# Performance work log

Hardware: AMD Instinct MI355X
Metric: run time of the kernel (lower is better)

The kernel has to match this reference:

```python
import jax, jax.numpy as jnp
import numpy as np

NUM_CLASSES = 2
BG_PID = 5532
NUM_ROIS = 128          # cfg.TRAIN.BATCH_SIZE
NUM_FG_MAX = 32         # round(cfg.TRAIN.FG_FRACTION * BATCH_SIZE), FG_FRACTION = 0.25
FG_THRESH = 0.5
BG_THRESH_HI = 0.5
BG_THRESH_LO = 0.1
MEANS = jnp.array([0.0, 0.0, 0.0, 0.0], dtype=jnp.float32)
STDS = jnp.array([0.1, 0.1, 0.2, 0.2], dtype=jnp.float32)
INSIDE_W = jnp.array([1.0, 1.0, 1.0, 1.0], dtype=jnp.float32)


def _make_boxes(key, n, img_w=1000.0, img_h=600.0):
    k1, k2, k3, k4 = jax.random.split(key, 4)
    x1 = jax.random.uniform(k1, (n,)) * (img_w - 330.0)
    y1 = jax.random.uniform(k2, (n,)) * (img_h - 350.0)
    w = 20.0 + jax.random.uniform(k3, (n,)) * 300.0
    h = 40.0 + jax.random.uniform(k4, (n,)) * 300.0
    return jnp.stack([x1, y1, x1 + w, y1 + h], axis=1).astype(jnp.float32)


def setup_inputs() -> dict:
    key = jax.random.key(0)
    kr, kg, kp = jax.random.split(key, 3)
    R, G = 131072, 256
    rois = _make_boxes(kr, R)
    all_rois = jnp.concatenate([jnp.zeros((R, 1), jnp.float32), rois], axis=1)  # [R,5]
    gtb = _make_boxes(kg, G)
    labels = jnp.ones((G, 1), jnp.float32)  # person class = 1
    pids = jax.random.randint(kp, (G, 1), 0, BG_PID).astype(jnp.float32)
    gt_boxes = jnp.concatenate([gtb, labels, pids], axis=1)  # [G,6]
    return {"all_rois": all_rois, "gt_boxes": gt_boxes}


def bbox_overlaps(a, b):
    iw = jnp.minimum(a[:, None, 2], b[None, :, 2]) - jnp.maximum(a[:, None, 0], b[None, :, 0]) + 1.0
    ih = jnp.minimum(a[:, None, 3], b[None, :, 3]) - jnp.maximum(a[:, None, 1], b[None, :, 1]) + 1.0
    iw = jnp.maximum(iw, 0.0)
    ih = jnp.maximum(ih, 0.0)
    area_a = (a[:, 2] - a[:, 0] + 1.0) * (a[:, 3] - a[:, 1] + 1.0)
    area_b = (b[:, 2] - b[:, 0] + 1.0) * (b[:, 3] - b[:, 1] + 1.0)
    inter = iw * ih
    return inter / (area_a[:, None] + area_b[None, :] - inter)


def bbox_transform(ex, gt):
    ew = ex[:, 2] - ex[:, 0] + 1.0
    eh = ex[:, 3] - ex[:, 1] + 1.0
    ecx = ex[:, 0] + 0.5 * ew
    ecy = ex[:, 1] + 0.5 * eh
    gw = gt[:, 2] - gt[:, 0] + 1.0
    gh = gt[:, 3] - gt[:, 1] + 1.0
    gcx = gt[:, 0] + 0.5 * gw
    gcy = gt[:, 1] + 0.5 * gh
    return jnp.stack([(gcx - ecx) / ew, (gcy - ecy) / eh,
                      jnp.log(gw / ew), jnp.log(gh / eh)], axis=1)


def _forward(all_rois, gt_boxes):
    G = gt_boxes.shape[0]
    gt_rois = jnp.concatenate([jnp.zeros((G, 1), all_rois.dtype), gt_boxes[:, :4]], axis=1)
    rois_all = jnp.concatenate([all_rois, gt_rois], axis=0)  # [R+G,5]
    N = rois_all.shape[0]
    overlaps = bbox_overlaps(rois_all[:, 1:5], gt_boxes[:, :4])  # [R+G, G]
    argmax_ov = jnp.argmax(overlaps, axis=1)
    max_ov = jnp.max(overlaps, axis=1)
    labels_all = gt_boxes[argmax_ov, 4]
    pids_all = gt_boxes[argmax_ov, 5]
    fg_mask = max_ov >= FG_THRESH
    bg_mask = (max_ov < BG_THRESH_HI) & (max_ov >= BG_THRESH_LO)
    num_fg = jnp.minimum(jnp.int32(NUM_FG_MAX), fg_mask.sum().astype(jnp.int32))
    num_bg = jnp.minimum(jnp.int32(NUM_ROIS) - num_fg, bg_mask.sum().astype(jnp.int32))
    # deterministic 'take first k' selection (DEBUG path of the original),
    # expressed as a fixed-shape scatter: rank within fg/bg -> output slot
    fg_rank = (jnp.cumsum(fg_mask) - 1).astype(jnp.int32)
    bg_rank = (jnp.cumsum(bg_mask) - 1).astype(jnp.int32)
    idx = jnp.arange(N, dtype=jnp.int32)
    pos_fg = jnp.where(fg_mask & (fg_rank < num_fg), fg_rank, jnp.int32(NUM_ROIS))
    pos_bg = jnp.where(bg_mask & (bg_rank < num_bg), num_fg + bg_rank, jnp.int32(NUM_ROIS))
    keep = jnp.zeros((NUM_ROIS,), jnp.int32)
    keep = keep.at[pos_fg].set(idx, mode="drop")
    keep = keep.at[pos_bg].set(idx, mode="drop")
    slot_is_fg = jnp.arange(NUM_ROIS) < num_fg
    rois = rois_all[keep]                                   # [128,5]
    labels = jnp.where(slot_is_fg, labels_all[keep], 0.0)
    pids = jnp.where(slot_is_fg, pids_all[keep], jnp.float32(BG_PID))
    tgt = bbox_transform(rois[:, 1:5], gt_boxes[argmax_ov[keep], :4])
    tgt = (tgt - MEANS) / STDS
    cls = jnp.round(labels).astype(jnp.int32)
    onehot = jax.nn.one_hot(cls, NUM_CLASSES, dtype=tgt.dtype) * (labels > 0).astype(tgt.dtype)[:, None]
    bbox_targets = (onehot[:, :, None] * tgt[:, None, :]).reshape(NUM_ROIS, 4 * NUM_CLASSES)
    bbox_inside = (onehot[:, :, None] * INSIDE_W[None, None, :]).reshape(NUM_ROIS, 4 * NUM_CLASSES)
    bbox_outside = (onehot[:, :, None] * jnp.ones((4,), tgt.dtype)).reshape(NUM_ROIS, 4 * NUM_CLASSES)
    return rois, labels, pids, bbox_targets, bbox_inside, bbox_outside


def reference(all_rois, gt_boxes):
    rois, labels, pids, bt, bi, bo = _forward(all_rois, gt_boxes)
    return rois, labels.astype(jnp.int32), pids.astype(jnp.int32), bt, bi, bo
```

## Files before the change

kernel.cpp:

```cpp
#include <hip/hip_runtime.h>
#include <stdint.h>

#define OUT_ROIS 128
#define FG_MAX 32
#define BG_PID_F 5532.0f
#define MAXCH 2304

#define MFG_D ((double)0x1FFFFFF / (double)(1 << 26))
#define MBG_D (26843545.0 / 268435456.0)

__global__ __launch_bounds__(512, 8) void ptl_classify(
    const float* __restrict__ all_rois, const float* __restrict__ gt,
    int R, int G, int N,
    uint8_t* __restrict__ code, int* __restrict__ blkF, int* __restrict__ blkB)
{
#pragma clang fp contract(off)
    __shared__ float4 g4[256];
    __shared__ float  gA[256];
    __shared__ uint32_t flg[4][128];
    const int t = threadIdx.x;
    const int w = t >> 6, lane = t & 63;
    const int q = w >> 1, half = w & 1;

    if (t < G) {
        const float* p = gt + (size_t)t * 6;
        const float a = p[0], b = p[1], c = p[2], d = p[3];
        g4[t] = make_float4(a, b, c, d);
        gA[t] = ((c - a) + 1.0f) * ((d - b) + 1.0f);
    }
    __syncthreads();

    const int rl = half * 64 + lane;
    const int i = blockIdx.x * 128 + rl;
    float x1, y1, x2, y2;
    if (i < N) {
        if (i < R) {
            const float* p = all_rois + (size_t)i * 5;
            x1 = p[1]; y1 = p[2]; x2 = p[3]; y2 = p[4];
        } else {
            const float* p = gt + (size_t)(i - R) * 6;
            x1 = p[0]; y1 = p[1]; x2 = p[2]; y2 = p[3];
        }
    } else { x1 = 0.0f; y1 = 0.0f; x2 = -2.0f; y2 = -2.0f; }
    const float A = ((x2 - x1) + 1.0f) * ((y2 - y1) + 1.0f);

    const int jbeg = (G * q) >> 2;
    const int jend = (G * (q + 1)) >> 2;
    double tF = 1.0, tB = 1.0;
#pragma unroll 8
    for (int j = jbeg; j < jend; ++j) {
        const float4 qq = g4[j];
        const float ga = gA[j];
        float iw = (fminf(x2, qq.z) - fmaxf(x1, qq.x)) + 1.0f;
        float ih = (fminf(y2, qq.w) - fmaxf(y1, qq.y)) + 1.0f;
        iw = fmaxf(iw, 0.0f);
        ih = fmaxf(ih, 0.0f);
        const float inter = iw * ih;
        const float den = (A + ga) - inter;
        const double i64 = (double)inter, d64 = (double)den;
        tF = fmin(tF, fma(MFG_D, d64, -i64));
        tB = fmin(tB, fma(MBG_D, d64, -i64));
    }
    flg[q][rl] = (tF <= 0.0 ? 1u : 0u) | (tB < 0.0 ? 2u : 0u);
    __syncthreads();

    if (t < 128) {
        const uint32_t u = flg[0][t] | flg[1][t] | flg[2][t] | flg[3][t];
        const int cls = (u & 1u) ? 1 : ((u & 2u) ? 2 : 0);
        const int i2 = blockIdx.x * 128 + t;
        if (i2 < N) code[i2] = (uint8_t)cls;
        unsigned long long mF = __ballot(cls == 1);
        unsigned long long mB = __ballot(cls == 2);
        if ((t & 63) == 0) {
            blkF[blockIdx.x * 2 + (t >> 6)] = __popcll(mF);
            blkB[blockIdx.x * 2 + (t >> 6)] = __popcll(mB);
        }
    }
}

__global__ __launch_bounds__(256) void ptl_select_emit(
    const float* __restrict__ all_rois, const float* __restrict__ gt,
    const uint8_t* __restrict__ code,
    const int* __restrict__ blkF, const int* __restrict__ blkB,
    int R, int G, int N, int nch,
    float* __restrict__ out)
{
#pragma clang fp contract(off)
    __shared__ int sF[MAXCH], sB[MAXCH];
    __shared__ int EF[MAXCH], EB[MAXCH];
    __shared__ int tsF[256], tsB[256];
    __shared__ int keep[OUT_ROIS];
    __shared__ int sam[OUT_ROIS];
    __shared__ int nwork;
    __shared__ unsigned short work[MAXCH];
    const int t = threadIdx.x;

    for (int c = t; c < nch; c += 256) { sF[c] = blkF[c]; sB[c] = blkB[c]; }
    for (int c = nch + t; c < MAXCH; c += 256) { sF[c] = 0; sB[c] = 0; }
    if (t < OUT_ROIS) { keep[t] = 0; sam[t] = 0; }
    if (t == 0) nwork = 0;
    __syncthreads();

    const int c0 = t * (MAXCH / 256);
    int baseF = 0, baseB = 0;
#pragma unroll
    for (int k = 0; k < MAXCH / 256; ++k) { baseF += sF[c0 + k]; baseB += sB[c0 + k]; }
    tsF[t] = baseF; tsB[t] = baseB;
    __syncthreads();
    for (int d = 1; d < 256; d <<= 1) {
        int vF = (t >= d) ? tsF[t - d] : 0;
        int vB = (t >= d) ? tsB[t - d] : 0;
        __syncthreads();
        tsF[t] += vF; tsB[t] += vB;
        __syncthreads();
    }
    const int tf = tsF[255], tb = tsB[255];
    const int num_fg = tf < FG_MAX ? tf : FG_MAX;
    const int rem = OUT_ROIS - num_fg;
    const int num_bg = tb < rem ? tb : rem;

    int rF = tsF[t] - baseF, rB = tsB[t] - baseB;
#pragma unroll
    for (int k = 0; k < MAXCH / 256; ++k) {
        const int c = c0 + k;
        const int cf = sF[c], cb = sB[c];
        EF[c] = rF; EB[c] = rB;
        const bool need = ((cf > 0 && rF < num_fg) || (cb > 0 && rB < num_bg)) && (c < nch);
        if (need) { int p = atomicAdd(&nwork, 1); work[p] = (unsigned short)c; }
        rF += cf; rB += cb;
    }
    __syncthreads();

    const int w = t >> 6, lane = t & 63;
    const unsigned long long lowmask = (1ull << lane) - 1ull;
    const int nw = nwork;
    for (int idx = w; idx < nw; idx += 4) {
        const int c = work[idx];
        const int i = c * 64 + lane;
        const int cd = (i < N) ? (int)code[i] : 0;
        unsigned long long mF = __ballot(cd == 1);
        unsigned long long mB = __ballot(cd == 2);
        const int pF = EF[c] + __popcll(mF & lowmask);
        const int pB = EB[c] + __popcll(mB & lowmask);
        if (cd == 1 && pF < num_fg) keep[pF] = i;
        if (cd == 2 && pB < num_bg) keep[num_fg + pB] = i;
    }
    __syncthreads();

    for (int s = w; s < num_fg; s += 4) {
        const int k = keep[s];
        float x1, y1, x2, y2;
        if (k < R) {
            const float* p = all_rois + (size_t)k * 5;
            x1 = p[1]; y1 = p[2]; x2 = p[3]; y2 = p[4];
        } else {
            const float* p = gt + (size_t)(k - R) * 6;
            x1 = p[0]; y1 = p[1]; x2 = p[2]; y2 = p[3];
        }
        const float A = ((x2 - x1) + 1.0f) * ((y2 - y1) + 1.0f);
        float mv = -1.0f; int mj = 0;
        for (int jj = 0; jj < 4; ++jj) {
            const int j = jj * 64 + lane;
            float iou = -1.0f;
            if (j < G) {
                const float* p = gt + (size_t)j * 6;
                const float a = p[0], b = p[1], c2 = p[2], d2 = p[3];
                const float ga = ((c2 - a) + 1.0f) * ((d2 - b) + 1.0f);
                float iw = (fminf(x2, c2) - fmaxf(x1, a)) + 1.0f;
                float ih = (fminf(y2, d2) - fmaxf(y1, b)) + 1.0f;
                iw = fmaxf(iw, 0.0f);
                ih = fmaxf(ih, 0.0f);
                const float inter = iw * ih;
                iou = inter / ((A + ga) - inter);
            }
            if (iou > mv) { mv = iou; mj = j; }
        }
#pragma unroll
        for (int m = 1; m < 64; m <<= 1) {
            const float ov = __shfl_xor(mv, m);
            const int oj = __shfl_xor(mj, m);
            if (ov > mv || (ov == mv && oj < mj)) { mv = ov; mj = oj; }
        }
        if (lane == 0) sam[s] = mj;
    }
    __syncthreads();

    if (t < OUT_ROIS) {
        const int s = t;
        const int k = keep[s];
        const bool isfg = s < num_fg;
        float x1, y1, x2, y2;
        if (k < R) {
            const float* p = all_rois + (size_t)k * 5;
            x1 = p[1]; y1 = p[2]; x2 = p[3]; y2 = p[4];
        } else {
            const float* p = gt + (size_t)(k - R) * 6;
            x1 = p[0]; y1 = p[1]; x2 = p[2]; y2 = p[3];
        }
        const int amax = sam[s];
        const float* g = gt + (size_t)amax * 6;
        const float gx1v = g[0], gy1v = g[1], gx2v = g[2], gy2v = g[3];
        const float label = isfg ? g[4] : 0.0f;
        const float pid = isfg ? g[5] : BG_PID_F;

        float* ro = out + (size_t)s * 5;
        ro[0] = 0.0f; ro[1] = x1; ro[2] = y1; ro[3] = x2; ro[4] = y2;
        out[640 + s] = (float)(int)label;
        out[768 + s] = (float)(int)pid;

        const float ew = (x2 - x1) + 1.0f, eh = (y2 - y1) + 1.0f;
        const float ecx = x1 + 0.5f * ew, ecy = y1 + 0.5f * eh;
        const float gw = (gx2v - gx1v) + 1.0f, gh = (gy2v - gy1v) + 1.0f;
        const float gcx = gx1v + 0.5f * gw, gcy = gy1v + 0.5f * gh;
        float tv[4];
        tv[0] = ((gcx - ecx) / ew) / 0.1f;
        tv[1] = ((gcy - ecy) / eh) / 0.1f;
        tv[2] = logf(gw / ew) / 0.2f;
        tv[3] = logf(gh / eh) / 0.2f;

        const int cls = (int)roundf(label);
        const float on = (label > 0.0f) ? 1.0f : 0.0f;

        float* bt = out + 896  + (size_t)s * 8;
        float* bi = out + 1920 + (size_t)s * 8;
        float* bo = out + 2944 + (size_t)s * 8;
#pragma unroll
        for (int cc = 0; cc < 2; ++cc) {
            const float sel = (cc == cls) ? on : 0.0f;
#pragma unroll
            for (int j = 0; j < 4; ++j) {
                bt[cc * 4 + j] = sel * tv[j];
                bi[cc * 4 + j] = sel;
                bo[cc * 4 + j] = sel;
            }
        }
    }
}

extern "C" void kernel_launch(void* const* d_in, const int* in_sizes, int n_in,
                              void* d_out, int out_size, void* d_ws, size_t ws_size,
                              hipStream_t stream) {
    const float* all_rois = (const float*)d_in[0];
    const float* gt       = (const float*)d_in[1];
    const int R = in_sizes[0] / 5;
    const int G = in_sizes[1] / 6;
    const int N = R + G;
    const int nblk = (N + 127) / 128;
    const int nch = (N + 63) / 64;

    uint8_t* code = (uint8_t*)d_ws;
    size_t codeBytes = ((size_t)N + 255) & ~(size_t)255;
    int* blkF = (int*)((char*)d_ws + codeBytes);
    int* blkB = blkF + 2 * nblk;
    float* out = (float*)d_out;

    ptl_classify<<<nblk, 512, 0, stream>>>(all_rois, gt, R, G, N, code, blkF, blkB);
    ptl_select_emit<<<1, 256, 0, stream>>>(all_rois, gt, code, blkF, blkB, R, G, N, nch, out);
}
```

Baseline: 44.13 us.

## Replace double-precision IoU threshold test with float FMA form, two rois per thread

The classify kernel swaps the per-pair double-precision fma/fmin threshold test for a single-precision sequence that splits each threshold constant into a main part plus a tiny correction term. Each thread now handles two rois against a 64-gt slice, which halves the block to 256 threads and reuses every shared-memory gt load for two rois. The goal is to remove the slow FP64 conversions and FMAs from the hot N×G loop and to raise ILP. The risk is that the float split may classify boxes at the exact 0.5/0.1 boundaries differently from the reference, and the gt loop is now hardcoded to 4×64 entries, which assumes G=256.

```diff
diff --git a/kernel.cpp b/kernel.cpp
--- a/kernel.cpp
+++ b/kernel.cpp
@@ -6,10 +6,8 @@
 #define BG_PID_F 5532.0f
 #define MAXCH 2304
 
-#define MFG_D ((double)0x1FFFFFF / (double)(1 << 26))
-#define MBG_D (26843545.0 / 268435456.0)
-
-__global__ __launch_bounds__(512, 8) void ptl_classify(
+
+__global__ __launch_bounds__(256, 4) void ptl_classify(
     const float* __restrict__ all_rois, const float* __restrict__ gt,
     int R, int G, int N,
     uint8_t* __restrict__ code, int* __restrict__ blkF, int* __restrict__ blkB)
@@ -17,10 +15,9 @@
 #pragma clang fp contract(off)
     __shared__ float4 g4[256];
     __shared__ float  gA[256];
-    __shared__ uint32_t flg[4][128];
+    __shared__ uint8_t flg[4][128];
     const int t = threadIdx.x;
     const int w = t >> 6, lane = t & 63;
-    const int q = w >> 1, half = w & 1;
 
     if (t < G) {
         const float* p = gt + (size_t)t * 6;
@@ -30,44 +27,63 @@
     }
     __syncthreads();
 
-    const int rl = half * 64 + lane;
-    const int i = blockIdx.x * 128 + rl;
-    float x1, y1, x2, y2;
-    if (i < N) {
-        if (i < R) {
-            const float* p = all_rois + (size_t)i * 5;
-            x1 = p[1]; y1 = p[2]; x2 = p[3]; y2 = p[4];
-        } else {
-            const float* p = gt + (size_t)(i - R) * 6;
-            x1 = p[0]; y1 = p[1]; x2 = p[2]; y2 = p[3];
-        }
-    } else { x1 = 0.0f; y1 = 0.0f; x2 = -2.0f; y2 = -2.0f; }
-    const float A = ((x2 - x1) + 1.0f) * ((y2 - y1) + 1.0f);
-
-    const int jbeg = (G * q) >> 2;
-    const int jend = (G * (q + 1)) >> 2;
-    double tF = 1.0, tB = 1.0;
-#pragma unroll 8
-    for (int j = jbeg; j < jend; ++j) {
-        const float4 qq = g4[j];
+    const int base = blockIdx.x * 128;
+    float x1a, y1a, x2a, y2a, x1b, y1b, x2b, y2b;
+    {
+        const int i0 = base + lane;
+        if (i0 < N) {
+            if (i0 < R) { const float* p = all_rois + (size_t)i0 * 5; x1a=p[1]; y1a=p[2]; x2a=p[3]; y2a=p[4]; }
+            else        { const float* p = gt + (size_t)(i0 - R) * 6; x1a=p[0]; y1a=p[1]; x2a=p[2]; y2a=p[3]; }
+        } else { x1a=0.0f; y1a=0.0f; x2a=-2.0f; y2a=-2.0f; }
+        const int i1 = base + 64 + lane;
+        if (i1 < N) {
+            if (i1 < R) { const float* p = all_rois + (size_t)i1 * 5; x1b=p[1]; y1b=p[2]; x2b=p[3]; y2b=p[4]; }
+            else        { const float* p = gt + (size_t)(i1 - R) * 6; x1b=p[0]; y1b=p[1]; x2b=p[2]; y2b=p[3]; }
+        } else { x1b=0.0f; y1b=0.0f; x2b=-2.0f; y2b=-2.0f; }
+    }
+    const float Aa = ((x2a - x1a) + 1.0f) * ((y2a - y1a) + 1.0f);
+    const float Ab = ((x2b - x1b) + 1.0f) * ((y2b - y1b) + 1.0f);
+
+    const int jbeg = w * 64;
+    float aF0 = -1e38f, aB0 = -1e38f, aF1 = -1e38f, aB1 = -1e38f;
+#pragma unroll 4
+    for (int jj = 0; jj < 64; ++jj) {
+        const int j = jbeg + jj;
+        const float4 q = g4[j];
         const float ga = gA[j];
-        float iw = (fminf(x2, qq.z) - fmaxf(x1, qq.x)) + 1.0f;
-        float ih = (fminf(y2, qq.w) - fmaxf(y1, qq.y)) + 1.0f;
-        iw = fmaxf(iw, 0.0f);
-        ih = fmaxf(ih, 0.0f);
-        const float inter = iw * ih;
-        const float den = (A + ga) - inter;
-        const double i64 = (double)inter, d64 = (double)den;
-        tF = fmin(tF, fma(MFG_D, d64, -i64));
-        tB = fmin(tB, fma(MBG_D, d64, -i64));
-    }
-    flg[q][rl] = (tF <= 0.0 ? 1u : 0u) | (tB < 0.0 ? 2u : 0u);
+        {
+            float iw = (fminf(x2a, q.z) - fmaxf(x1a, q.x)) + 1.0f;
+            float ih = (fminf(y2a, q.w) - fmaxf(y1a, q.y)) + 1.0f;
+            iw = fmaxf(iw, 0.0f); ih = fmaxf(ih, 0.0f);
+            const float I = iw * ih;
+            const float D = (Aa + ga) - I;
+            const float h  = fmaf(-0.5f, D, I);
+            const float gF = fmaf(0x1p-26f, D, h);
+            const float h2 = fmaf(-0.1f, D, I);
+            const float gB = fmaf(0x1p-28f, D, h2);
+            aF0 = fmaxf(aF0, gF); aB0 = fmaxf(aB0, gB);
+        }
+        {
+            float iw = (fminf(x2b, q.z) - fmaxf(x1b, q.x)) + 1.0f;
+            float ih = (fminf(y2b, q.w) - fmaxf(y1b, q.y)) + 1.0f;
+            iw = fmaxf(iw, 0.0f); ih = fmaxf(ih, 0.0f);
+            const float I = iw * ih;
+            const float D = (Ab + ga) - I;
+            const float h  = fmaf(-0.5f, D, I);
+            const float gF = fmaf(0x1p-26f, D, h);
+            const float h2 = fmaf(-0.1f, D, I);
+            const float gB = fmaf(0x1p-28f, D, h2);
+            aF1 = fmaxf(aF1, gF); aB1 = fmaxf(aB1, gB);
+        }
+    }
+    flg[w][lane]      = (uint8_t)((aF0 >= 0.0f ? 1u : 0u) | (aB0 > 0.0f ? 2u : 0u));
+    flg[w][64 + lane] = (uint8_t)((aF1 >= 0.0f ? 1u : 0u) | (aB1 > 0.0f ? 2u : 0u));
     __syncthreads();
 
     if (t < 128) {
-        const uint32_t u = flg[0][t] | flg[1][t] | flg[2][t] | flg[3][t];
+        const uint32_t u = (uint32_t)flg[0][t] | flg[1][t] | flg[2][t] | flg[3][t];
         const int cls = (u & 1u) ? 1 : ((u & 2u) ? 2 : 0);
-        const int i2 = blockIdx.x * 128 + t;
+        const int i2 = base + t;
         if (i2 < N) code[i2] = (uint8_t)cls;
         unsigned long long mF = __ballot(cls == 1);
         unsigned long long mB = __ballot(cls == 2);
@@ -150,13 +166,8 @@
     for (int s = w; s < num_fg; s += 4) {
         const int k = keep[s];
         float x1, y1, x2, y2;
-        if (k < R) {
-            const float* p = all_rois + (size_t)k * 5;
-            x1 = p[1]; y1 = p[2]; x2 = p[3]; y2 = p[4];
-        } else {
-            const float* p = gt + (size_t)(k - R) * 6;
-            x1 = p[0]; y1 = p[1]; x2 = p[2]; y2 = p[3];
-        }
+        if (k < R) { const float* p = all_rois + (size_t)k * 5; x1=p[1]; y1=p[2]; x2=p[3]; y2=p[4]; }
+        else       { const float* p = gt + (size_t)(k - R) * 6; x1=p[0]; y1=p[1]; x2=p[2]; y2=p[3]; }
         const float A = ((x2 - x1) + 1.0f) * ((y2 - y1) + 1.0f);
         float mv = -1.0f; int mj = 0;
         for (int jj = 0; jj < 4; ++jj) {
@@ -168,8 +179,7 @@
                 const float ga = ((c2 - a) + 1.0f) * ((d2 - b) + 1.0f);
                 float iw = (fminf(x2, c2) - fmaxf(x1, a)) + 1.0f;
                 float ih = (fminf(y2, d2) - fmaxf(y1, b)) + 1.0f;
-                iw = fmaxf(iw, 0.0f);
-                ih = fmaxf(ih, 0.0f);
+                iw = fmaxf(iw, 0.0f); ih = fmaxf(ih, 0.0f);
                 const float inter = iw * ih;
                 iou = inter / ((A + ga) - inter);
             }
@@ -190,13 +200,8 @@
         const int k = keep[s];
         const bool isfg = s < num_fg;
         float x1, y1, x2, y2;
-        if (k < R) {
-            const float* p = all_rois + (size_t)k * 5;
-            x1 = p[1]; y1 = p[2]; x2 = p[3]; y2 = p[4];
-        } else {
-            const float* p = gt + (size_t)(k - R) * 6;
-            x1 = p[0]; y1 = p[1]; x2 = p[2]; y2 = p[3];
-        }
+        if (k < R) { const float* p = all_rois + (size_t)k * 5; x1=p[1]; y1=p[2]; x2=p[3]; y2=p[4]; }
+        else       { const float* p = gt + (size_t)(k - R) * 6; x1=p[0]; y1=p[1]; x2=p[2]; y2=p[3]; }
         const int amax = sam[s];
         const float* g = gt + (size_t)amax * 6;
         const float gx1v = g[0], gy1v = g[1], gx2v = g[2], gy2v = g[3];
@@ -254,6 +259,6 @@
     int* blkB = blkF + 2 * nblk;
     float* out = (float*)d_out;
 
-    ptl_classify<<<nblk, 512, 0, stream>>>(all_rois, gt, R, G, N, code, blkF, blkB);
+    ptl_classify<<<nblk, 256, 0, stream>>>(all_rois, gt, R, G, N, code, blkF, blkB);
     ptl_select_emit<<<1, 256, 0, stream>>>(all_rois, gt, code, blkF, blkB, R, G, N, nch, out);
 }
```

Result: faster. 38.43 us (-12.9%).
